# Kernel tuning notes

Measured on AMD Instinct MI355X. Metric: run time of the kernel, lower is better.

## Reference

```python
import jax, jax.numpy as jnp
import numpy as np

C = 768
H = 12
B = 4
T = 16
K = 196


def _ln(x, g, b, eps=1e-5):
    mu = jnp.mean(x, axis=-1, keepdims=True)
    var = jnp.mean(jnp.square(x - mu), axis=-1, keepdims=True)
    return (x - mu) / jnp.sqrt(var + eps) * g + b


def _mha(x, Wq, bq, Wk, bk, Wv, bv):
    # x: [b, n, c]; standard multi-head attention, scale = head_dim**-0.5
    b, n, c = x.shape
    hd = c // H
    scale = hd ** -0.5
    def heads(y):
        return y.reshape(b, n, H, hd).transpose(0, 2, 1, 3)  # b h n d
    q = heads(x @ Wq + bq)
    k = heads(x @ Wk + bk)
    v = heads(x @ Wv + bv)
    a = jax.nn.softmax(jnp.einsum('bhqd,bhkd->bhqk', q, k) * scale, axis=-1)
    o = jnp.einsum('bhqk,bhkd->bhqd', a, v)
    return o.transpose(0, 2, 1, 3).reshape(b, n, c)


def setup_inputs() -> dict:
    key = jax.random.key(0)
    ks = jax.random.split(key, 8)
    M = T * K + 1
    w = lambda k, shape: jax.random.normal(k, shape, dtype=jnp.float32) * 0.02
    return {
        'x': jax.random.normal(ks[0], (B, M, C), dtype=jnp.float32),
        'ln1_g': jnp.ones((C,), jnp.float32), 'ln1_b': jnp.zeros((C,), jnp.float32),
        'tln_g': jnp.ones((C,), jnp.float32), 'tln_b': jnp.zeros((C,), jnp.float32),
        'ln2_g': jnp.ones((C,), jnp.float32), 'ln2_b': jnp.zeros((C,), jnp.float32),
        'Ws': w(ks[1], (4, C, C)), 'bs': jnp.zeros((4, C), jnp.float32),
        'Wt': w(ks[2], (9, C, C)), 'bt': jnp.zeros((9, C), jnp.float32),
        'Wtp': w(ks[3], (3, C, C)), 'btp': jnp.zeros((3, C), jnp.float32),
        'Wfc': w(ks[4], (C, C)), 'bfc': jnp.zeros((C,), jnp.float32),
        'W1': w(ks[5], (C, 4 * C)), 'b1': jnp.zeros((4 * C,), jnp.float32),
        'W2': w(ks[6], (4 * C, C)), 'b2': jnp.zeros((C,), jnp.float32),
        'T': T, 'K': K,
    }


def reference(x, ln1_g, ln1_b, tln_g, tln_b, ln2_g, ln2_b, Ws, bs, Wt, bt, Wtp, btp, Wfc, bfc, W1, b1, W2, b2, T, K):
    Bsz, M, Cd = x.shape
    t1, t2 = T // 4, T // 2
    # ---- temporal branch: 'b (k t) c -> (b k) t c' ----
    xt = x[:, 1:].reshape(Bsz * K, T, Cd)
    h = _ln(xt, tln_g, tln_b)
    # three windowed temporal scales
    o4 = _mha(h[:, T - t1:], Wt[0], bt[0], Wt[1], bt[1], Wt[2], bt[2])
    o8 = _mha(h[:, t2:], Wt[3], bt[3], Wt[4], bt[4], Wt[5], bt[5])
    o16 = _mha(h, Wt[6], bt[6], Wt[7], bt[7], Wt[8], bt[8])
    o4 = o4 @ Wtp[0] + btp[0]
    o8 = o8.at[:, t1:].set(0.5 * o8[:, t1:] + 0.5 * o4)
    o8 = o8 @ Wtp[1] + btp[1]
    o16 = o16.at[:, t2:].set(0.5 * o16[:, t2:] + 0.5 * o8)
    o16 = o16 @ Wtp[2] + btp[2]
    res_temporal = o16.reshape(Bsz, K * T, Cd)  # '(b k) t c -> b (k t) c'
    xt2 = res_temporal @ Wfc + bfc + x[:, 1:]
    # ---- spatial branch: 'b (k t) c -> (b t) k c' with cls prepended ----
    init_cls = x[:, :1]  # [B,1,C]
    cls = jnp.broadcast_to(init_cls, (Bsz, T, Cd)).reshape(Bsz * T, 1, Cd)
    xs = xt2.reshape(Bsz, K, T, Cd).transpose(0, 2, 1, 3).reshape(Bsz * T, K, Cd)
    xs = jnp.concatenate([cls, xs], axis=1)  # [(B T), K+1, C]
    hs = _ln(xs, ln1_g, ln1_b)
    os_ = _mha(hs, Ws[0], bs[0], Ws[1], bs[1], Ws[2], bs[2]) @ Ws[3] + bs[3]
    cls_out = os_[:, 0].reshape(Bsz, T, Cd).mean(axis=1, keepdims=True)
    res_spatial = os_[:, 1:].reshape(Bsz, T, K, Cd).transpose(0, 2, 1, 3).reshape(Bsz, K * T, Cd)
    xn = jnp.concatenate([init_cls, xt2], axis=1) + jnp.concatenate([cls_out, res_spatial], axis=1)
    # ---- MLP ----
    h2 = _ln(xn, ln2_g, ln2_b)
    mlp = jax.nn.gelu(h2 @ W1 + b1, approximate=False) @ W2 + b2
    return xn + mlp
```

## Files before the change

kernel.cpp:

```cpp
#include <hip/hip_runtime.h>

typedef unsigned short u16;
typedef unsigned int   u32;
typedef __attribute__((ext_vector_type(8))) __bf16 bf16x8;
typedef __attribute__((ext_vector_type(4))) float  f32x4;
typedef __attribute__((ext_vector_type(4))) u16    u16x4;

#define DEV __device__ __forceinline__

DEV float bf2f(u16 u){ union { u32 i; float f; } x; x.i = ((u32)u) << 16; return x.f; }
DEV u16 f2bf(float f){ union { float f; u32 i; } x; x.f = f;
  u32 r = x.i + 0x7fffu + ((x.i >> 16) & 1u); return (u16)(r >> 16); }

DEV void gload16(const void* g, void* l){
  __builtin_amdgcn_global_load_lds((const __attribute__((address_space(1))) void*)g,
                                   (__attribute__((address_space(3))) void*)l, 16, 0, 0);
}

__global__ __launch_bounds__(256)
void twt_k(const float* __restrict__ src, u16* __restrict__ dst, int R, int C){
  __shared__ float t[32][33];
  int tx = threadIdx.x & 31, ty = threadIdx.x >> 5;
  int c0 = blockIdx.x * 32, r0 = blockIdx.y * 32;
  #pragma unroll
  for (int i = 0; i < 4; i++)
    t[ty + i*8][tx] = src[(size_t)(r0 + ty + i*8) * C + c0 + tx];
  __syncthreads();
  #pragma unroll
  for (int i = 0; i < 4; i++)
    dst[(size_t)(c0 + ty + i*8) * R + r0 + tx] = f2bf(t[tx][ty + i*8]);
}

__global__ __launch_bounds__(256)
void twt17_k(const float* __restrict__ Ws, const float* __restrict__ Wt,
             const float* __restrict__ Wtp, const float* __restrict__ Wfc,
             u16* __restrict__ dst){
  __shared__ float t[32][33];
  int z = blockIdx.z;
  const float* src = (z < 4)  ? Ws  + (size_t)z * 589824
                   : (z < 13) ? Wt  + (size_t)(z-4) * 589824
                   : (z < 16) ? Wtp + (size_t)(z-13) * 589824
                   : Wfc;
  u16* d = dst + (size_t)z * 589824;
  int tx = threadIdx.x & 31, ty = threadIdx.x >> 5;
  int c0 = blockIdx.x * 32, r0 = blockIdx.y * 32;
  #pragma unroll
  for (int i = 0; i < 4; i++)
    t[ty + i*8][tx] = src[(size_t)(r0 + ty + i*8) * 768 + c0 + tx];
  __syncthreads();
  #pragma unroll
  for (int i = 0; i < 4; i++)
    d[(size_t)(c0 + ty + i*8) * 768 + r0 + tx] = f2bf(t[tx][ty + i*8]);
}

__global__ void fillz_k(u32* __restrict__ p, long n){
  long i = (long)blockIdx.x * 256 + threadIdx.x;
  long stride = (long)gridDim.x * 256;
  for (; i < n; i += stride) p[i] = 0;
}

template<int GM>
__global__ __launch_bounds__(256)
void ln_k(const float* __restrict__ f0, const u16* __restrict__ b0_,
          const float* __restrict__ gw, const float* __restrict__ bw,
          u16* __restrict__ out){
  int lane = threadIdx.x & 63;
  int tok = blockIdx.x * 4 + (threadIdx.x >> 6);
  const float* fsrc = nullptr; const u16* bsrc = nullptr;
  bool bfp = false;
  if constexpr (GM == 0){
    int b = tok / 3136, m = tok - b * 3136;
    fsrc = f0 + ((size_t)b * 3137 + 1 + m) * 768;
  } else if constexpr (GM == 1){
    int s = tok / 197, j = tok - s * 197;
    int b = s >> 4, t = s & 15;
    if (j == 0) fsrc = f0 + (size_t)b * 3137 * 768;
    else { bfp = true; bsrc = b0_ + ((size_t)b * 3136 + (size_t)(j - 1) * 16 + t) * 768; }
  } else {
    fsrc = f0 + (size_t)tok * 768;
  }
  float v[12]; float s1 = 0.f, s2 = 0.f;
  if (!bfp){
    #pragma unroll
    for (int i = 0; i < 3; i++){
      float4 f = *(const float4*)(fsrc + i * 256 + lane * 4);
      v[i*4+0] = f.x; v[i*4+1] = f.y; v[i*4+2] = f.z; v[i*4+3] = f.w;
    }
  } else {
    #pragma unroll
    for (int i = 0; i < 3; i++){
      u16x4 p = *(const u16x4*)(bsrc + i * 256 + lane * 4);
      v[i*4+0] = bf2f(p[0]); v[i*4+1] = bf2f(p[1]); v[i*4+2] = bf2f(p[2]); v[i*4+3] = bf2f(p[3]);
    }
  }
  #pragma unroll
  for (int i = 0; i < 12; i++){ s1 += v[i]; s2 += v[i]*v[i]; }
  #pragma unroll
  for (int off = 32; off; off >>= 1){ s1 += __shfl_xor(s1, off); s2 += __shfl_xor(s2, off); }
  float mu = s1 * (1.f/768.f);
  float rstd = rsqrtf(s2 * (1.f/768.f) - mu*mu + 1e-5f);
  #pragma unroll
  for (int i = 0; i < 3; i++){
    int c = i * 256 + lane * 4;
    float4 g4 = *(const float4*)(gw + c);
    float4 b4 = *(const float4*)(bw + c);
    u16x4 pk;
    pk[0] = f2bf((v[i*4+0]-mu)*rstd*g4.x + b4.x);
    pk[1] = f2bf((v[i*4+1]-mu)*rstd*g4.y + b4.y);
    pk[2] = f2bf((v[i*4+2]-mu)*rstd*g4.z + b4.z);
    pk[3] = f2bf((v[i*4+3]-mu)*rstd*g4.w + b4.w);
    *(u16x4*)(out + (size_t)tok * 768 + c) = pk;
  }
}

template<int MODE>
__global__ __launch_bounds__(256, 4)
void gemm_k(const u16* __restrict__ A, const u16* __restrict__ Bw,
            const float* __restrict__ bias, void* out,
            const void* aux1, void* aux2, int nbx,
            int M, int K, int lda, int ldo,
            int aTs, int aTf, int at0, int oTs, int oTf, int ot0){
  __shared__ u16 lA[2][128 * 32];
  __shared__ u16 lB[2][128 * 32];
  const int tid = threadIdx.x;

  const int nwg = (int)gridDim.x;
  int id = (int)blockIdx.x;
  int qc = nwg >> 3, rc = nwg & 7;
  int xcd = id & 7, off = id >> 3;
  int wg = (xcd < rc ? xcd * (qc + 1) : rc * (qc + 1) + (xcd - rc) * qc) + off;
  int by = wg / nbx;
  int bx = wg - by * nbx;
  const int m0 = by * 128, n0 = bx * 128;

  const int lane = tid & 63, widx = tid >> 6;
  const int g = lane >> 4, r16 = lane & 15;
  const int wm = widx >> 1, wn = widx & 1;

  const u16* ga0; const u16* ga1; const u16* gb0; const u16* gb1;
  u32 lo0, lo1;
  {
    int li = tid;
    int ar = m0 + (li >> 2); if (ar > M - 1) ar = M - 1;
    ar = (ar / aTs) * aTf + at0 + (ar % aTs);
    ga0 = A + (size_t)ar * lda + (li & 3) * 8;
    gb0 = Bw + (size_t)(n0 + (li >> 2)) * K + (li & 3) * 8;
    lo0 = li * 8;
    li = tid + 256;
    ar = m0 + (li >> 2); if (ar > M - 1) ar = M - 1;
    ar = (ar / aTs) * aTf + at0 + (ar % aTs);
    ga1 = A + (size_t)ar * lda + (li & 3) * 8;
    gb1 = Bw + (size_t)(n0 + (li >> 2)) * K + (li & 3) * 8;
    lo1 = li * 8;
  }

  const f32x4 vz = {0.f, 0.f, 0.f, 0.f};
  f32x4 acc[4][4];
  #pragma unroll
  for (int i = 0; i < 4; i++)
    #pragma unroll
    for (int j = 0; j < 4; j++) acc[i][j] = vz;

  const int kiter = K >> 5;

  gload16(ga0, &lA[0][lo0]);
  gload16(ga1, &lA[0][lo1]);
  gload16(gb0, &lB[0][lo0]);
  gload16(gb1, &lB[0][lo1]);
  ga0 += 32; ga1 += 32; gb0 += 32; gb1 += 32;
  __syncthreads();

  for (int kt = 0; kt < kiter; ++kt){
    const int cur = kt & 1;
    if (kt + 1 < kiter){
      const int nxt = cur ^ 1;
      gload16(ga0, &lA[nxt][lo0]);
      gload16(ga1, &lA[nxt][lo1]);
      gload16(gb0, &lB[nxt][lo0]);
      gload16(gb1, &lB[nxt][lo1]);
      ga0 += 32; ga1 += 32; gb0 += 32; gb1 += 32;
    }
    bf16x8 af[4], bfr[4];
    #pragma unroll
    for (int i = 0; i < 4; i++){
      af[i]  = *(const bf16x8*)(&lA[cur][(wm * 64 + i * 16 + r16) * 32 + g * 8]);
      bfr[i] = *(const bf16x8*)(&lB[cur][(wn * 64 + i * 16 + r16) * 32 + g * 8]);
    }
    #pragma unroll
    for (int i = 0; i < 4; i++)
      #pragma unroll
      for (int j = 0; j < 4; j++)
        acc[i][j] = __builtin_amdgcn_mfma_f32_16x16x32_bf16(af[i], bfr[j], acc[i][j], 0, 0, 0);
    __syncthreads();
  }

  #pragma unroll
  for (int i = 0; i < 4; i++){
    const int lrow = wm * 64 + i * 16 + g * 4;
    #pragma unroll
    for (int j = 0; j < 4; j++){
      const int Cg = n0 + wn * 64 + j * 16 + r16;
      const float b0 = bias[Cg];
      float vv[4];
      #pragma unroll
      for (int r = 0; r < 4; r++) vv[r] = acc[i][j][r] + b0;

      if constexpr (MODE == 8){
        int mat = Cg / 768, c0 = Cg - mat * 768;
        if (mat < 2){
          #pragma unroll
          for (int r = 0; r < 4; r++){
            int R = m0 + lrow + r;
            if (R < M)
              ((u16*)out)[(size_t)mat * ot0 * 768 + (size_t)R * 768 + c0] = f2bf(vv[r]);
          }
        } else {
          int R0 = m0 + lrow;
          if (R0 < M){
            int seq_ = R0 / oTs, t0 = R0 - seq_ * oTs;
            u16x4 pk;
            #pragma unroll
            for (int r = 0; r < 4; r++) pk[r] = f2bf(vv[r]);
            *(u16x4*)((u16*)aux2 +
              ((size_t)(seq_ * 12 + (c0 >> 6)) * 64 + (c0 & 63)) * ldo + t0) = pk;
          }
        }
      } else if constexpr (MODE == 9){
        int mat = Cg / 768, c0 = Cg - mat * 768;
        if (mat < 2){
          #pragma unroll
          for (int r = 0; r < 4; r++){
            int R = m0 + lrow + r;
            if (R < M)
              ((u16*)out)[(size_t)mat * ot0 * 768 + (size_t)R * 768 + c0] = f2bf(vv[r]);
          }
        } else {
          int R0 = m0 + lrow;
          if (R0 < M){
            int s_ = R0 / 197, j0 = R0 - s_ * 197;
            if (j0 <= 193){
              u16x4 pk;
              #pragma unroll
              for (int r = 0; r < 4; r++) pk[r] = f2bf(vv[r]);
              *(u16x4*)((u16*)aux2 +
                ((size_t)(s_ * 12 + (c0 >> 6)) * 64 + (c0 & 63)) * 224 + j0 + (s_ & 3)) = pk;
            } else {
              #pragma unroll
              for (int r = 0; r < 4; r++){
                int R = R0 + r;
                if (R < M){
                  int s2 = R / 197, j2 = R - s2 * 197;
                  ((u16*)aux2)[((size_t)(s2 * 12 + (c0 >> 6)) * 64 + (c0 & 63)) * 224
                               + j2 + (s2 & 3)] = f2bf(vv[r]);
                }
              }
            }
          }
        }
      } else {
        #pragma unroll
        for (int r = 0; r < 4; r++){
          const int R = m0 + lrow + r;
          if (R >= M) continue;
          float val = vv[r];
          if constexpr (MODE == 0){
            ((u16*)out)[(size_t)R * ldo + Cg] = f2bf(val);
          } else if constexpr (MODE == 1){
            int Ro = (R / oTs) * oTf + ot0 + (R % oTs);
            u16* po = (u16*)out + (size_t)Ro * ldo + Cg;
            *po = f2bf(0.5f * val + 0.5f * bf2f(*po));
          } else if constexpr (MODE == 2){
            int b_ = R / 3136, m_ = R - b_ * 3136;
            ((u16*)out)[(size_t)R * 768 + Cg] =
                f2bf(val + ((const float*)aux1)[((size_t)b_ * 3137 + 1 + m_) * 768 + Cg]);
          } else if constexpr (MODE == 3){
            int s_ = R / 197, j_ = R - s_ * 197;
            if (j_ == 0){
              ((float*)aux2)[(size_t)s_ * 768 + Cg] = val;
            } else {
              int b_ = s_ >> 4, t_ = s_ & 15, m_ = (j_ - 1) * 16 + t_;
              ((float*)out)[((size_t)b_ * 3137 + 1 + m_) * 768 + Cg] =
                  val + bf2f(((const u16*)aux1)[((size_t)b_ * 3136 + m_) * 768 + Cg]);
            }
          } else if constexpr (MODE == 4){
            float c = val * (0.7978845608f + 0.0356774081f * val * val);
            float e2 = __expf(2.f * fabsf(c));
            float th = __builtin_copysignf(1.f - 2.f / (e2 + 1.f), c);
            ((u16*)out)[(size_t)R * ldo + Cg] = f2bf(0.5f * val * (1.f + th));
          } else if constexpr (MODE == 5){
            ((float*)out)[(size_t)R * 768 + Cg] = val + ((const float*)aux1)[(size_t)R * 768 + Cg];
          }
        }
      }
    }
  }
}

template<int TS, int TSPAD>
__global__ __launch_bounds__(256)
void tattn_k(const u16* __restrict__ q, const u16* __restrict__ k,
             const u16* __restrict__ vt, u16* __restrict__ o){
  const int lane = threadIdx.x & 63;
  const int g = lane >> 4, r16 = lane & 15;
  int p = blockIdx.x * 4 + (threadIdx.x >> 6);
  int seq = p / 12, h = p - seq * 12;

  int trow = (TS < 16 && r16 >= TS) ? TS - 1 : r16;
  size_t qko = (size_t)(seq * TS + trow) * 768 + h * 64 + g * 8;
  bf16x8 ak0 = *(const bf16x8*)(k + qko);
  bf16x8 ak1 = *(const bf16x8*)(k + qko + 32);
  bf16x8 bq0 = *(const bf16x8*)(q + qko);
  bf16x8 bq1 = *(const bf16x8*)(q + qko + 32);

  f32x4 s = {0.f, 0.f, 0.f, 0.f};
  s = __builtin_amdgcn_mfma_f32_16x16x32_bf16(ak0, bq0, s, 0, 0, 0);
  s = __builtin_amdgcn_mfma_f32_16x16x32_bf16(ak1, bq1, s, 0, 0, 0);

  const float C = 0.125f * 1.44269504089f;
  float pv[4]; float mx = -3e38f;
  #pragma unroll
  for (int r = 0; r < 4; r++){
    float x = (g * 4 + r < TS) ? s[r] : -3e38f;
    pv[r] = x; mx = fmaxf(mx, x);
  }
  mx = fmaxf(mx, __shfl_xor(mx, 16));
  mx = fmaxf(mx, __shfl_xor(mx, 32));
  float sum = 0.f;
  #pragma unroll
  for (int r = 0; r < 4; r++){ pv[r] = exp2f((pv[r] - mx) * C); sum += pv[r]; }
  sum += __shfl_xor(sum, 16);
  sum += __shfl_xor(sum, 32);
  float inv = 1.f / sum;
  #pragma unroll
  for (int r = 0; r < 4; r++) pv[r] *= inv;

  u32 w0 = (u32)f2bf(pv[0]) | ((u32)f2bf(pv[1]) << 16);
  u32 w1 = (u32)f2bf(pv[2]) | ((u32)f2bf(pv[3]) << 16);
  int a0 = ((g * 2) * 16 + r16) * 4;
  int a1 = ((g * 2 + 1) * 16 + r16) * 4;
  u32 msk = (g < 2) ? 0xFFFFFFFFu : 0u;
  union { u32 w[4]; bf16x8 v; } pa;
  pa.w[0] = msk & (u32)__builtin_amdgcn_ds_bpermute(a0, (int)w0);
  pa.w[1] = msk & (u32)__builtin_amdgcn_ds_bpermute(a0, (int)w1);
  pa.w[2] = msk & (u32)__builtin_amdgcn_ds_bpermute(a1, (int)w0);
  pa.w[3] = msk & (u32)__builtin_amdgcn_ds_bpermute(a1, (int)w1);

  const u16* vb = vt + ((size_t)(seq * 12 + h) * 64) * TSPAD;
  const f32x4 vz = {0.f, 0.f, 0.f, 0.f};
  f32x4 oc[4];
  #pragma unroll
  for (int dt = 0; dt < 4; ++dt){
    bf16x8 bv = *(const bf16x8*)(vb + (size_t)(dt * 16 + r16) * TSPAD + g * 8);
    oc[dt] = __builtin_amdgcn_mfma_f32_16x16x32_bf16(pa.v, bv, vz, 0, 0, 0);
  }
  #pragma unroll
  for (int rr = 0; rr < 4; ++rr){
    int qr = g * 4 + rr;
    if (qr < TS){
      size_t ob = (size_t)(seq * TS + qr) * 768 + h * 64 + r16;
      #pragma unroll
      for (int dt = 0; dt < 4; ++dt)
        o[ob + dt * 16] = f2bf(oc[dt][rr]);
    }
  }
}

__global__ __launch_bounds__(64)
void sattn_k(const u16* __restrict__ qs, const u16* __restrict__ ks,
             const u16* __restrict__ vt, u16* __restrict__ o){
  __shared__ u16 Pl[16 * 224];
  const int lane = threadIdx.x & 63;
  const int g = lane >> 4, r16 = lane & 15;
  int bid = blockIdx.x;
  int chunk = bid % 13; int sh_ = bid / 13;
  int h = sh_ % 12, s = sh_ / 12;
  const int shft = s & 3;
  const float sc_l2e = 0.125f * 1.44269504089f;

  #pragma unroll
  for (int i = 0; i < 4; i++){
    Pl[(i * 4 + g) * 224 + 208 + r16] = 0;
    if (r16 < 4) Pl[(i * 4 + g) * 224 + r16] = 0;
  }

  int q0 = chunk * 16;
  int qrow = q0 + r16; if (qrow > 196) qrow = 196;
  const u16* qp = qs + ((size_t)(s * 197 + qrow)) * 768 + h * 64 + g * 8;
  bf16x8 aq0 = *(const bf16x8*)qp;
  bf16x8 aq1 = *(const bf16x8*)(qp + 32);

  f32x4 scv[13];
  #pragma unroll
  for (int jt = 0; jt < 13; ++jt){
    int krow = jt * 16 + r16; if (krow > 196) krow = 196;
    const u16* kp = ks + ((size_t)(s * 197 + krow)) * 768 + h * 64 + g * 8;
    bf16x8 b0 = *(const bf16x8*)kp;
    bf16x8 b1 = *(const bf16x8*)(kp + 32);
    f32x4 z = {0.f, 0.f, 0.f, 0.f};
    z = __builtin_amdgcn_mfma_f32_16x16x32_bf16(aq0, b0, z, 0, 0, 0);
    z = __builtin_amdgcn_mfma_f32_16x16x32_bf16(aq1, b1, z, 0, 0, 0);
    scv[jt] = z;
  }
  float mrow[4] = {-3e38f, -3e38f, -3e38f, -3e38f};
  #pragma unroll
  for (int jt = 0; jt < 13; ++jt)
    #pragma unroll
    for (int r = 0; r < 4; r++){
      float x = (jt * 16 + r16 < 197) ? scv[jt][r] : -3e38f;
      scv[jt][r] = x;
      mrow[r] = fmaxf(mrow[r], x);
    }
  #pragma unroll
  for (int off = 1; off < 16; off <<= 1)
    #pragma unroll
    for (int r = 0; r < 4; r++) mrow[r] = fmaxf(mrow[r], __shfl_xor(mrow[r], off));
  float srow[4] = {0.f, 0.f, 0.f, 0.f};
  #pragma unroll
  for (int jt = 0; jt < 13; ++jt)
    #pragma unroll
    for (int r = 0; r < 4; r++){
      float e = exp2f((scv[jt][r] - mrow[r]) * sc_l2e);
      scv[jt][r] = e;
      srow[r] += e;
    }
  #pragma unroll
  for (int off = 1; off < 16; off <<= 1)
    #pragma unroll
    for (int r = 0; r < 4; r++) srow[r] += __shfl_xor(srow[r], off);
  float inv[4];
  #pragma unroll
  for (int r = 0; r < 4; r++) inv[r] = 1.f / srow[r];
  #pragma unroll
  for (int jt = 0; jt < 13; ++jt)
    #pragma unroll
    for (int r = 0; r < 4; r++)
      Pl[(g * 4 + r) * 224 + jt * 16 + r16 + shft] = f2bf(scv[jt][r] * inv[r]);
  __syncthreads();
  const u16* vbase = vt + ((size_t)(s * 12 + h) * 64) * 224;
  f32x4 oc[4]; const f32x4 vz = {0.f,0.f,0.f,0.f};
  #pragma unroll
  for (int dt = 0; dt < 4; dt++) oc[dt] = vz;
  #pragma unroll
  for (int ks2 = 0; ks2 < 7; ++ks2){
    bf16x8 ap = *(const bf16x8*)(Pl + r16 * 224 + ks2 * 32 + g * 8);
    #pragma unroll
    for (int dt = 0; dt < 4; ++dt){
      const u16* vp = vbase + ((size_t)(dt * 16 + r16)) * 224 + ks2 * 32 + g * 8;
      bf16x8 bv = *(const bf16x8*)vp;
      oc[dt] = __builtin_amdgcn_mfma_f32_16x16x32_bf16(ap, bv, oc[dt], 0, 0, 0);
    }
  }
  #pragma unroll
  for (int dt = 0; dt < 4; ++dt)
    #pragma unroll
    for (int r = 0; r < 4; r++){
      int qr2 = q0 + g * 4 + r;
      if (qr2 < 197)
        o[((size_t)(s * 197 + qr2)) * 768 + h * 64 + dt * 16 + r16] = f2bf(oc[dt][r]);
    }
}

__global__ __launch_bounds__(256)
void clsfin_k(const float* __restrict__ x, const float* __restrict__ cb, float* __restrict__ xn){
  int b = blockIdx.x;
  int c = blockIdx.y * 256 + threadIdx.x;
  float s = 0.f;
  #pragma unroll
  for (int t = 0; t < 16; t++) s += cb[((size_t)(b * 16 + t)) * 768 + c];
  xn[(size_t)b * 3137 * 768 + c] = x[(size_t)b * 3137 * 768 + c] + s * (1.f / 16.f);
}

extern "C" void kernel_launch(void* const* d_in, const int* in_sizes, int n_in,
                              void* d_out, int out_size, void* d_ws, size_t ws_size,
                              hipStream_t stream){
  (void)in_sizes; (void)n_in; (void)out_size;
  const float* x    = (const float*)d_in[0];
  const float* ln1g = (const float*)d_in[1];
  const float* ln1b = (const float*)d_in[2];
  const float* tlng = (const float*)d_in[3];
  const float* tlnb = (const float*)d_in[4];
  const float* ln2g = (const float*)d_in[5];
  const float* ln2b = (const float*)d_in[6];
  const float* Ws   = (const float*)d_in[7];
  const float* bs   = (const float*)d_in[8];
  const float* Wt   = (const float*)d_in[9];
  const float* bt   = (const float*)d_in[10];
  const float* Wtp  = (const float*)d_in[11];
  const float* btp  = (const float*)d_in[12];
  const float* Wfc  = (const float*)d_in[13];
  const float* bfc  = (const float*)d_in[14];
  const float* W1   = (const float*)d_in[15];
  const float* b1   = (const float*)d_in[16];
  const float* W2   = (const float*)d_in[17];
  const float* b2   = (const float*)d_in[18];
  float* out = (float*)d_out;

  constexpr size_t MiB = 1048576;
  constexpr size_t C2  = 589824;
  constexpr size_t W_BYTES = (17 * C2 + 2 * 2359296) * 2;
  constexpr size_t NEED = W_BYTES + 143 * MiB;
  if (ws_size < NEED) return;

  char* wsb  = (char*)d_ws;
  u16*  wbuf = (u16*)wsb;
  u16*  W1T  = wbuf + 17 * C2;
  u16*  W2T  = W1T + (size_t)3072 * 768;
  char* A0   = wsb + W_BYTES;

  u16*  ht  = (u16*)(A0 + 0   * MiB);
  u16*  qk  = (u16*)(A0 + 20  * MiB);
  u16*  vtb = (u16*)(A0 + 58  * MiB);
  u16*  o16 = (u16*)(A0 + 86  * MiB);
  u16*  o8  = (u16*)(A0 + 105 * MiB);
  u16*  o4  = (u16*)(A0 + 115 * MiB);
  u16*  xt2 = (u16*)(A0 + 86  * MiB);
  float* xn = (float*)(A0 + 105 * MiB);
  float* clsb = (float*)(A0 + 142 * MiB);
  u16*  tp  = qk;
  u16*  hs  = ht;  u16* osb = ht; u16* h2 = ht;
  u16*  a1  = qk;

  twt17_k<<<dim3(24, 24, 17), 256, 0, stream>>>(Ws, Wt, Wtp, Wfc, wbuf);
  twt_k<<<dim3(96, 24), 256, 0, stream>>>(W1, W1T, 768, 3072);
  twt_k<<<dim3(24, 96), 256, 0, stream>>>(W2, W2T, 3072, 768);

  ln_k<0><<<3136, 256, 0, stream>>>(x, nullptr, tlng, tlnb, ht);

  gemm_k<8><<<18*98, 256, 0, stream>>>(ht, wbuf + 10*C2, bt + 6*768, qk, nullptr, vtb, 18, 12544, 768, 768, 24, 1,1,0, 16,1,12544);
  tattn_k<16,24><<<2352, 256, 0, stream>>>(qk, qk + (size_t)12544*768, vtb, o16);

  gemm_k<8><<<18*49, 256, 0, stream>>>(ht, wbuf +  7*C2, bt + 3*768, qk, nullptr, vtb, 18, 6272, 768, 768, 16, 8,16,8, 8,1,6272);
  tattn_k< 8,16><<<2352, 256, 0, stream>>>(qk, qk + (size_t)6272*768, vtb, o8);

  gemm_k<8><<<18*25, 256, 0, stream>>>(ht, wbuf +  4*C2, bt + 0*768, qk, nullptr, vtb, 18, 3136, 768, 768, 16, 4,16,12, 4,1,3136);
  tattn_k< 4,16><<<2352, 256, 0, stream>>>(qk, qk + (size_t)3136*768, vtb, o4);

  gemm_k<1><<<6*25, 256, 0, stream>>>(o4,  wbuf + 13*C2, btp + 0,    o8,  nullptr, nullptr, 6, 3136, 768, 768, 768, 1,1,0, 4,8,4);
  gemm_k<1><<<6*49, 256, 0, stream>>>(o8,  wbuf + 14*C2, btp + 768,  o16, nullptr, nullptr, 6, 6272, 768, 768, 768, 1,1,0, 8,16,8);
  gemm_k<0><<<6*98, 256, 0, stream>>>(o16, wbuf + 15*C2, btp + 1536, tp,  nullptr, nullptr, 6, 12544, 768, 768, 768, 1,1,0, 1,1,0);
  gemm_k<2><<<6*98, 256, 0, stream>>>(tp,  wbuf + 16*C2, bfc,        xt2, x, nullptr,       6, 12544, 768, 768, 768, 1,1,0, 1,1,0);

  ln_k<1><<<3152, 256, 0, stream>>>(x, xt2, ln1g, ln1b, hs);
  fillz_k<<<2048, 256, 0, stream>>>((u32*)vtb, 5505024);
  gemm_k<9><<<18*99, 256, 0, stream>>>(hs, wbuf + 0*C2, bs + 0, qk, nullptr, vtb, 18, 12608, 768, 768, 224, 1,1,0, 1,1,12608);

  sattn_k<<<9984, 64, 0, stream>>>(qk, qk + (size_t)12608*768, vtb, osb);

  gemm_k<3><<<6*99, 256, 0, stream>>>(osb, wbuf + 3*C2, bs + 2304, xn, xt2, clsb, 6, 12608, 768, 768, 768, 1,1,0, 1,1,0);
  clsfin_k<<<dim3(4, 3), 256, 0, stream>>>(x, clsb, xn);

  ln_k<2><<<3137, 256, 0, stream>>>(xn, nullptr, ln2g, ln2b, h2);
  gemm_k<4><<<24*99, 256, 0, stream>>>(h2, W1T, b1, a1,  nullptr, nullptr, 24, 12548, 768, 768, 3072, 1,1,0, 1,1,0);
  gemm_k<5><<<6*99, 256, 0, stream>>>(a1, W2T, b2, out, xn, nullptr,       6, 12548, 3072, 3072, 768, 1,1,0, 1,1,0);
}
```

Measured before the change: 723.0 us.

## Fold Wtp[2] and Wfc projections into one precomputed weight matrix

Two consecutive linear projections (o16 @ Wtp[2] + btp[2], then @ Wfc + bfc) are merged by precomputing the product Wtp[2]·Wfc and the combined bias on device at call time. This drops one 12544x768x768 GEMM and its intermediate buffer write and read, at the cost of a small 768^3 weight GEMM, a conversion kernel and a bias-prep kernel per call. The product is formed in bf16, so the fused weight carries different rounding than applying the two projections in sequence, and several workspace buffers are relocated to make room.

```diff
diff --git a/kernel.cpp b/kernel.cpp
--- a/kernel.cpp
+++ b/kernel.cpp
@@ -51,6 +51,25 @@
   #pragma unroll
   for (int i = 0; i < 4; i++)
     d[(size_t)(c0 + ty + i*8) * 768 + r0 + tx] = f2bf(t[tx][ty + i*8]);
+}
+
+__global__ __launch_bounds__(256)
+void cvt_k(const float* __restrict__ src, u16* __restrict__ dst){
+  int i = (blockIdx.x * 256 + threadIdx.x) * 4;
+  float4 f = *(const float4*)(src + i);
+  u16x4 p; p[0] = f2bf(f.x); p[1] = f2bf(f.y); p[2] = f2bf(f.z); p[3] = f2bf(f.w);
+  *(u16x4*)(dst + i) = p;
+}
+
+__global__ __launch_bounds__(256)
+void bprep_k(const float* __restrict__ btp2, const float* __restrict__ Wfc,
+             const float* __restrict__ bfc, float* __restrict__ bprime,
+             float* __restrict__ zb){
+  int n = blockIdx.x * 256 + threadIdx.x;
+  float acc = bfc[n];
+  for (int k = 0; k < 768; k++) acc += btp2[k] * Wfc[(size_t)k * 768 + n];
+  bprime[n] = acc;
+  zb[n] = 0.f;
 }
 
 __global__ void fillz_k(u32* __restrict__ p, long n){
@@ -513,16 +532,22 @@
   u16*  o16 = (u16*)(A0 + 86  * MiB);
   u16*  o8  = (u16*)(A0 + 105 * MiB);
   u16*  o4  = (u16*)(A0 + 115 * MiB);
-  u16*  xt2 = (u16*)(A0 + 86  * MiB);
-  float* xn = (float*)(A0 + 105 * MiB);
+  u16*  xt2 = (u16*)(A0 + 105 * MiB);
+  float* xn = (float*)(A0 + 20 * MiB);
+  u16*  wtp2b = (u16*)(A0 + 132 * MiB);
+  u16*  WpT   = (u16*)(A0 + 134 * MiB);
+  float* bprime = (float*)(A0 + 136 * MiB);
+  float* zb     = bprime + 1024;
   float* clsb = (float*)(A0 + 142 * MiB);
-  u16*  tp  = qk;
   u16*  hs  = ht;  u16* osb = ht; u16* h2 = ht;
-  u16*  a1  = qk;
+  u16*  a1  = (u16*)(A0 + 58 * MiB);
 
   twt17_k<<<dim3(24, 24, 17), 256, 0, stream>>>(Ws, Wt, Wtp, Wfc, wbuf);
   twt_k<<<dim3(96, 24), 256, 0, stream>>>(W1, W1T, 768, 3072);
   twt_k<<<dim3(24, 96), 256, 0, stream>>>(W2, W2T, 3072, 768);
+  cvt_k<<<576, 256, 0, stream>>>(Wtp + 2 * 589824, wtp2b);
+  bprep_k<<<3, 256, 0, stream>>>(btp + 1536, Wfc, bfc, bprime, zb);
+  gemm_k<0><<<36, 256, 0, stream>>>(wbuf + 16*C2, wtp2b, zb, WpT, nullptr, nullptr, 6, 768, 768, 768, 768, 1,1,0, 1,1,0);
 
   ln_k<0><<<3136, 256, 0, stream>>>(x, nullptr, tlng, tlnb, ht);
 
@@ -537,8 +562,7 @@
 
   gemm_k<1><<<6*25, 256, 0, stream>>>(o4,  wbuf + 13*C2, btp + 0,    o8,  nullptr, nullptr, 6, 3136, 768, 768, 768, 1,1,0, 4,8,4);
   gemm_k<1><<<6*49, 256, 0, stream>>>(o8,  wbuf + 14*C2, btp + 768,  o16, nullptr, nullptr, 6, 6272, 768, 768, 768, 1,1,0, 8,16,8);
-  gemm_k<0><<<6*98, 256, 0, stream>>>(o16, wbuf + 15*C2, btp + 1536, tp,  nullptr, nullptr, 6, 12544, 768, 768, 768, 1,1,0, 1,1,0);
-  gemm_k<2><<<6*98, 256, 0, stream>>>(tp,  wbuf + 16*C2, bfc,        xt2, x, nullptr,       6, 12544, 768, 768, 768, 1,1,0, 1,1,0);
+  gemm_k<2><<<6*98, 256, 0, stream>>>(o16, WpT,          bprime,     xt2, x, nullptr,       6, 12544, 768, 768, 768, 1,1,0, 1,1,0);
 
   ln_k<1><<<3152, 256, 0, stream>>>(x, xt2, ln1g, ln1b, hs);
   fillz_k<<<2048, 256, 0, stream>>>((u32*)vtb, 5505024);
```

Measured after the change: 763.8 us. +5.6%, slower.
